# Kernel tuning notes

Measured on AMD Instinct MI355X. Metric: run time of the kernel, lower is better.

## Reference

```python
import jax, jax.numpy as jnp
import numpy as np

N_NODES = 50000
N_EDGES = 800000
NUM_GRAPHS = 64
EPS = 1e-5


def setup_inputs() -> dict:
    key = jax.random.key(0)
    ks = jax.random.split(key, 24)
    d = {}
    d['x'] = jax.random.normal(ks[0], (N_NODES, 128), dtype=jnp.float32)
    d['edge_index'] = jax.random.randint(ks[1], (2, N_EDGES), 0, N_NODES, dtype=jnp.int32)
    d['batch'] = jnp.sort(jax.random.randint(ks[2], (N_NODES,), 0, NUM_GRAPHS, dtype=jnp.int32))
    def w(k, shape, fan_in):
        return jax.random.normal(k, shape, dtype=jnp.float32) * (1.0 / np.sqrt(fan_in))
    d['W1'] = w(ks[3], (128, 256), 128)
    d['asrc1'] = w(ks[4], (4, 64), 64)
    d['adst1'] = w(ks[5], (4, 64), 64)
    d['b1'] = jnp.zeros((256,), jnp.float32)
    d['g1'] = jnp.ones((256,), jnp.float32)
    d['be1'] = jnp.zeros((256,), jnp.float32)
    d['W2'] = w(ks[6], (256, 256), 256)
    d['asrc2'] = w(ks[7], (4, 64), 64)
    d['adst2'] = w(ks[8], (4, 64), 64)
    d['b2'] = jnp.zeros((256,), jnp.float32)
    d['g2'] = jnp.ones((256,), jnp.float32)
    d['be2'] = jnp.zeros((256,), jnp.float32)
    d['W3'] = w(ks[9], (256, 128), 256)
    d['asrc3'] = w(ks[10], (1, 128), 128)
    d['adst3'] = w(ks[11], (1, 128), 128)
    d['b3'] = jnp.zeros((128,), jnp.float32)
    d['g3'] = jnp.ones((128,), jnp.float32)
    d['be3'] = jnp.zeros((128,), jnp.float32)
    d['Wp'] = w(ks[12], (256, 128), 256)
    d['bp'] = jnp.zeros((128,), jnp.float32)
    return d


def _gat(x, src, dst, W, a_src, a_dst, b, concat):
    # PyG GATConv: shared linear, per-edge additive attention, segment softmax over dst
    N = x.shape[0]
    H, C = a_src.shape
    xl = (x @ W).reshape(N, H, C)                       # [N,H,C]
    a_l = jnp.sum(xl * a_src[None], axis=-1)            # [N,H]
    a_r = jnp.sum(xl * a_dst[None], axis=-1)            # [N,H]
    e = jax.nn.leaky_relu(a_l[src] + a_r[dst], 0.2)     # [E,H]
    m = jax.ops.segment_max(e, dst, num_segments=N)
    m = jnp.where(jnp.isfinite(m), m, 0.0)
    p = jnp.exp(e - m[dst])
    s = jax.ops.segment_sum(p, dst, num_segments=N)
    alpha = p / (s[dst] + 1e-16)                        # [E,H]
    out = jax.ops.segment_sum(alpha[:, :, None] * xl[src], dst, num_segments=N)  # [N,H,C]
    out = out.reshape(N, H * C) if concat else out.mean(axis=1)
    return out + b


def _ln(x, g, b):
    mu = x.mean(-1, keepdims=True)
    var = x.var(-1, keepdims=True)
    return (x - mu) * jax.lax.rsqrt(var + EPS) * g + b


def reference(x, edge_index, batch, W1, asrc1, adst1, b1, g1, be1,
              W2, asrc2, adst2, b2, g2, be2,
              W3, asrc3, adst3, b3, g3, be3, Wp, bp):
    N = x.shape[0]
    loops = jnp.arange(N, dtype=edge_index.dtype)
    src = jnp.concatenate([edge_index[0], loops])  # add_self_loops=True
    dst = jnp.concatenate([edge_index[1], loops])
    h = jax.nn.relu(_ln(_gat(x, src, dst, W1, asrc1, adst1, b1, True), g1, be1))
    h = jax.nn.relu(_ln(_gat(h, src, dst, W2, asrc2, adst2, b2, True), g2, be2))
    h = jax.nn.relu(_ln(_gat(h, src, dst, W3, asrc3, adst3, b3, False), g3, be3))
    cnt = jax.ops.segment_sum(jnp.ones((N,), h.dtype), batch, num_segments=NUM_GRAPHS)
    h_mean = jax.ops.segment_sum(h, batch, num_segments=NUM_GRAPHS) / jnp.maximum(cnt, 1.0)[:, None]
    h_max = jax.ops.segment_max(h, batch, num_segments=NUM_GRAPHS)
    g = jnp.concatenate([h_mean, h_max], axis=-1)       # [B, 2*embed]
    return g @ Wp + bp
```

## Files before the change

kernel.cpp:

```cpp
#include <hip/hip_runtime.h>

#define EPS_LN 1e-5f
typedef unsigned int uint;

using bf16x8 = __attribute__((ext_vector_type(8))) short;
using f32x4  = __attribute__((ext_vector_type(4))) float;

__device__ inline float bf2f(ushort h){ return __uint_as_float(((uint)h) << 16); }
__device__ inline ushort f2bf(float f){
  uint u = __float_as_uint(f);
  u += 0x7fffu + ((u >> 16) & 1u);
  return (ushort)(u >> 16);
}

__global__ void k_deg(const int* __restrict__ ei, int* __restrict__ deg, int E, int N){
  int e = blockIdx.x * 256 + threadIdx.x;
  if (e >= E + N) return;
  int dst = (e < E) ? ei[E + e] : (e - E);
  atomicAdd(&deg[dst], 1);
}

__global__ __launch_bounds__(1024) void k_bsum(const int* __restrict__ deg, int* __restrict__ bsum, int n){
  __shared__ int ws[16];
  const int t = (int)threadIdx.x, lane = t & 63, w = t >> 6;
  int i = blockIdx.x * 1024 + t;
  int v = (i < n) ? deg[i] : 0;
  #pragma unroll
  for (int off = 32; off; off >>= 1) v += __shfl_xor(v, off);
  if (lane == 0) ws[w] = v;
  __syncthreads();
  if (t == 0){
    int s = 0;
    #pragma unroll
    for (int k = 0; k < 16; k++) s += ws[k];
    bsum[blockIdx.x] = s;
  }
}

__global__ __launch_bounds__(256) void k_misc(int* __restrict__ bsum, int nb,
                                              const int* __restrict__ batch, int* __restrict__ pos,
                                              int N, int G){
  const int t = (int)threadIdx.x;
  if (blockIdx.x == 0){
    if (t >= 64) return;
    const int lane = t;
    int carry = 0;
    for (int b0 = 0; b0 < nb; b0 += 64){
      int i = b0 + lane;
      int v = (i < nb) ? bsum[i] : 0;
      int s = v;
      #pragma unroll
      for (int off = 1; off < 64; off <<= 1){ int u = __shfl_up(s, off); if (lane >= off) s += u; }
      if (i < nb) bsum[i] = s - v + carry;
      carry += __shfl(s, 63);
    }
  } else {
    int g = t;
    if (g > G) return;
    int lo = 0, hi = N;
    while (lo < hi){
      int mid = (lo + hi) >> 1;
      if (batch[mid] < g) lo = mid + 1; else hi = mid;
    }
    pos[g] = lo;
  }
}

__global__ __launch_bounds__(1024) void k_scan2(const int* __restrict__ deg, const int* __restrict__ bpre,
                                                int* __restrict__ row_ptr, int* __restrict__ cursor, int n){
  __shared__ int wsum[16];
  const int t = (int)threadIdx.x, lane = t & 63, w = t >> 6;
  int i = blockIdx.x * 1024 + t;
  int v = (i < n) ? deg[i] : 0;
  int s = v;
  #pragma unroll
  for (int off = 1; off < 64; off <<= 1){ int u = __shfl_up(s, off); if (lane >= off) s += u; }
  if (lane == 63) wsum[w] = s;
  __syncthreads();
  if (w == 0 && lane < 16){
    int sc = wsum[lane];
    #pragma unroll
    for (int off = 1; off < 16; off <<= 1){ int u = __shfl_up(sc, off); if (lane >= off) sc += u; }
    wsum[lane] = sc;
  }
  __syncthreads();
  int prefix = bpre[blockIdx.x] + (w ? wsum[w - 1] : 0) + s;
  if (i < n){ row_ptr[i + 1] = prefix; cursor[i] = prefix - v; }
  if (i == 0) row_ptr[0] = 0;
}

__global__ void k_scatter(const int* __restrict__ ei, int* __restrict__ cursor,
                          int* __restrict__ csr_src, int E, int N){
  int e = blockIdx.x * 256 + threadIdx.x;
  if (e >= E + N) return;
  int src, dst;
  if (e < E){ src = ei[e]; dst = ei[E + e]; } else { src = dst = e - E; }
  int pos = atomicAdd(&cursor[dst], 1);
  csr_src[pos] = src;
}

__global__ void k_prep(const float* __restrict__ x, ushort* __restrict__ x_bf,
                       const float* __restrict__ W1, ushort* __restrict__ W1t,
                       const float* __restrict__ W2, ushort* __restrict__ W2t,
                       const float* __restrict__ W3, ushort* __restrict__ W3t, int N){
  int i = blockIdx.x * 256 + threadIdx.x;
  const int c0 = N * 32;
  if (i < c0){
    float4 v = reinterpret_cast<const float4*>(x)[i];
    ushort4 o; o.x = f2bf(v.x); o.y = f2bf(v.y); o.z = f2bf(v.z); o.w = f2bf(v.w);
    reinterpret_cast<ushort4*>(x_bf)[i] = o;
    return;
  }
  i -= c0;
  if (i < 256 * 128){
    int n = i >> 7, k = i & 127;
    W1t[i] = f2bf(W1[(size_t)k * 256 + n]);
    return;
  }
  i -= 256 * 128;
  if (i < 256 * 256){
    int n = i >> 8, k = i & 255;
    W2t[i] = f2bf(W2[(size_t)k * 256 + n]);
    return;
  }
  i -= 256 * 256;
  if (i < 128 * 256){
    int n = i >> 8, k = i & 255;
    W3t[i] = f2bf(W3[(size_t)k * 128 + n]);
  }
}

template<int K, int N, int H>
__global__ __launch_bounds__(256, 2) void k_mm(const ushort* __restrict__ A,
                                               const ushort* __restrict__ Wt,
                                               ushort* __restrict__ out,
                                               const float* __restrict__ asrc,
                                               const float* __restrict__ adst,
                                               float* __restrict__ al, float* __restrict__ ar,
                                               int M)
{
  constexpr int BANDS = (N / H) / 64;
  __shared__ __align__(16) ushort ldsA[128 * 128];
  __shared__ __align__(16) ushort ldsB[128 * 128];

  const int t = (int)threadIdx.x;
  const int lane = t & 63;
  const int w = t >> 6;
  const int wm = w >> 1, wn = w & 1;
  const int row0 = blockIdx.x * 128;
  const int n0 = blockIdx.y * 128;
  const int trow = t >> 4;
  const int tk = t & 15;

  f32x4 acc[4][4];
  #pragma unroll
  for (int mt = 0; mt < 4; mt++)
    #pragma unroll
    for (int nt = 0; nt < 4; nt++)
      acc[mt][nt] = (f32x4){0.f, 0.f, 0.f, 0.f};

  #pragma unroll
  for (int kt = 0; kt < K / 128; kt++){
    uint4 ra[8], rb[8];
    #pragma unroll
    for (int p = 0; p < 8; p++){
      int arow = p * 16 + trow;
      int grow = row0 + arow; if (grow > M - 1) grow = M - 1;
      ra[p] = *reinterpret_cast<const uint4*>(&A[(size_t)grow * K + kt * 128 + tk * 8]);
      rb[p] = *reinterpret_cast<const uint4*>(&Wt[(size_t)(n0 + arow) * K + kt * 128 + tk * 8]);
    }
    if (kt) __syncthreads();
    #pragma unroll
    for (int p = 0; p < 8; p++){
      int arow = p * 16 + trow;
      int sw = (tk ^ (arow & 7)) * 8;
      *reinterpret_cast<uint4*>(&ldsA[arow * 128 + sw]) = ra[p];
      *reinterpret_cast<uint4*>(&ldsB[arow * 128 + sw]) = rb[p];
    }
    __syncthreads();

    #pragma unroll
    for (int ks = 0; ks < 4; ks++){
      bf16x8 af[4], bfr[4];
      const int kb8 = ks * 4 + (lane >> 4);
      #pragma unroll
      for (int mt = 0; mt < 4; mt++){
        int arow = wm * 64 + mt * 16 + (lane & 15);
        af[mt] = *reinterpret_cast<const bf16x8*>(&ldsA[arow * 128 + ((kb8 ^ (arow & 7)) * 8)]);
        int brow = wn * 64 + mt * 16 + (lane & 15);
        bfr[mt] = *reinterpret_cast<const bf16x8*>(&ldsB[brow * 128 + ((kb8 ^ (brow & 7)) * 8)]);
      }
      #pragma unroll
      for (int mt = 0; mt < 4; mt++)
        #pragma unroll
        for (int nt = 0; nt < 4; nt++)
          acc[mt][nt] = __builtin_amdgcn_mfma_f32_16x16x32_bf16(af[mt], bfr[nt], acc[mt][nt], 0, 0, 0);
    }
  }

  #pragma unroll
  for (int mt = 0; mt < 4; mt++){
    const int grow_b = row0 + wm * 64 + mt * 16 + (lane >> 4) * 4;
    #pragma unroll
    for (int nt = 0; nt < 4; nt++){
      const int gcol = n0 + wn * 64 + nt * 16 + (lane & 15);
      #pragma unroll
      for (int r = 0; r < 4; r++){
        int grow = grow_b + r;
        if (grow < M) out[(size_t)grow * N + gcol] = f2bf(acc[mt][nt][r]);
      }
    }
  }

  float av[4], bv[4];
  #pragma unroll
  for (int nt = 0; nt < 4; nt++){
    int col = n0 + wn * 64 + nt * 16 + (lane & 15);
    av[nt] = asrc[col]; bv[nt] = adst[col];
  }
  float paA[4][4], pbA[4][4];
  #pragma unroll
  for (int mt = 0; mt < 4; mt++){
    #pragma unroll
    for (int r = 0; r < 4; r++){
      float pa = acc[mt][0][r] * av[0] + acc[mt][1][r] * av[1]
               + acc[mt][2][r] * av[2] + acc[mt][3][r] * av[3];
      float pb = acc[mt][0][r] * bv[0] + acc[mt][1][r] * bv[1]
               + acc[mt][2][r] * bv[2] + acc[mt][3][r] * bv[3];
      #pragma unroll
      for (int off = 1; off < 16; off <<= 1){ pa += __shfl_xor(pa, off); pb += __shfl_xor(pb, off); }
      paA[mt][r] = pa; pbA[mt][r] = pb;
    }
  }
  if constexpr (BANDS == 1){
    const int h = (n0 + wn * 64) / (N / H);
    if ((lane & 15) == 0){
      #pragma unroll
      for (int mt = 0; mt < 4; mt++){
        #pragma unroll
        for (int r = 0; r < 4; r++){
          int row = row0 + wm * 64 + mt * 16 + (lane >> 4) * 4 + r;
          if (row < M){
            al[(size_t)row * H + h] = paA[mt][r];
            ar[(size_t)row * H + h] = pbA[mt][r];
          }
        }
      }
    }
  } else {
    __syncthreads();
    float* fl = reinterpret_cast<float*>(ldsA);
    if (wn == 0 && (lane & 15) == 0){
      #pragma unroll
      for (int mt = 0; mt < 4; mt++){
        #pragma unroll
        for (int r = 0; r < 4; r++){
          int rl = wm * 64 + mt * 16 + (lane >> 4) * 4 + r;
          fl[rl] = paA[mt][r]; fl[128 + rl] = pbA[mt][r];
        }
      }
    }
    __syncthreads();
    if (wn == 1 && (lane & 15) == 0){
      #pragma unroll
      for (int mt = 0; mt < 4; mt++){
        #pragma unroll
        for (int r = 0; r < 4; r++){
          int rl = wm * 64 + mt * 16 + (lane >> 4) * 4 + r;
          int row = row0 + rl;
          if (row < M){
            al[row] = fl[rl] + paA[mt][r];
            ar[row] = fl[128 + rl] + pbA[mt][r];
          }
        }
      }
    }
  }
}

template<int DIM>
__device__ inline void gstep4(const char* __restrict__ xlb, int laneB, int s, float p, float* acc){
  uint2 v = *reinterpret_cast<const uint2*>(xlb + (size_t)((uint)s * (uint)(DIM * 2)) + laneB);
  acc[0] = fmaf(p, __uint_as_float(v.x << 16), acc[0]);
  acc[1] = fmaf(p, __uint_as_float(v.x & 0xffff0000u), acc[1]);
  acc[2] = fmaf(p, __uint_as_float(v.y << 16), acc[2]);
  acc[3] = fmaf(p, __uint_as_float(v.y & 0xffff0000u), acc[3]);
}
template<int DIM>
__device__ inline void gstep2(const char* __restrict__ xlb, int laneB, int s, float p, float* acc){
  uint v = *reinterpret_cast<const uint*>(xlb + (size_t)((uint)s * (uint)(DIM * 2)) + laneB);
  acc[0] = fmaf(p, __uint_as_float(v << 16), acc[0]);
  acc[1] = fmaf(p, __uint_as_float(v & 0xffff0000u), acc[1]);
}

template<int H, int DIM, bool BF16_OUT>
__global__ __launch_bounds__(256) void k_aggw(
    const ushort* __restrict__ xl,
    const float* __restrict__ al, const float* __restrict__ ar,
    const int* __restrict__ row_ptr, const int* __restrict__ csr_src,
    const float* __restrict__ bias, const float* __restrict__ gamma, const float* __restrict__ beta,
    float* __restrict__ out, int N)
{
  constexpr int EPL = DIM / 64;
  constexpr int PST = 68;
  const int tid = (int)threadIdx.x;
  const int wid = tid >> 6, lane = tid & 63;
  __shared__ float plds_all[4][H * PST];
  __shared__ int   slds_all[4][64];
  float* plds = plds_all[wid];
  int*   slds = slds_all[wid];
  const int n = blockIdx.x * 4 + wid;
  if (n >= N) return;
  const int start = __builtin_amdgcn_readfirstlane(row_ptr[n]);
  const int end   = __builtin_amdgcn_readfirstlane(row_ptr[n + 1]);
  const int deg   = end - start;
  const int hm    = (H == 4) ? (lane >> 4) : 0;
  const int hb    = hm * PST;
  const int laneB = lane * (EPL * 2);

  float arv[H];
  #pragma unroll
  for (int h = 0; h < H; h++) arv[h] = ar[(size_t)n * H + h];

  float acc[EPL];
  #pragma unroll
  for (int e = 0; e < EPL; e++) acc[e] = 0.f;
  float psum[H];
  const char* xlb = (const char*)xl;

  auto gather = [&](int cnt){
    int j = 0;
    for (; j + 8 <= cnt; j += 8){
      int s0 = slds[j+0], s1 = slds[j+1], s2 = slds[j+2], s3 = slds[j+3];
      int s4 = slds[j+4], s5 = slds[j+5], s6 = slds[j+6], s7 = slds[j+7];
      float q0 = plds[hb+j+0], q1 = plds[hb+j+1], q2 = plds[hb+j+2], q3 = plds[hb+j+3];
      float q4 = plds[hb+j+4], q5 = plds[hb+j+5], q6 = plds[hb+j+6], q7 = plds[hb+j+7];
      if constexpr (EPL == 4){
        gstep4<DIM>(xlb, laneB, s0, q0, acc); gstep4<DIM>(xlb, laneB, s1, q1, acc);
        gstep4<DIM>(xlb, laneB, s2, q2, acc); gstep4<DIM>(xlb, laneB, s3, q3, acc);
        gstep4<DIM>(xlb, laneB, s4, q4, acc); gstep4<DIM>(xlb, laneB, s5, q5, acc);
        gstep4<DIM>(xlb, laneB, s6, q6, acc); gstep4<DIM>(xlb, laneB, s7, q7, acc);
      } else {
        gstep2<DIM>(xlb, laneB, s0, q0, acc); gstep2<DIM>(xlb, laneB, s1, q1, acc);
        gstep2<DIM>(xlb, laneB, s2, q2, acc); gstep2<DIM>(xlb, laneB, s3, q3, acc);
        gstep2<DIM>(xlb, laneB, s4, q4, acc); gstep2<DIM>(xlb, laneB, s5, q5, acc);
        gstep2<DIM>(xlb, laneB, s6, q6, acc); gstep2<DIM>(xlb, laneB, s7, q7, acc);
      }
    }
    for (; j + 2 <= cnt; j += 2){
      int s0 = slds[j+0], s1 = slds[j+1];
      float q0 = plds[hb+j+0], q1 = plds[hb+j+1];
      if constexpr (EPL == 4){ gstep4<DIM>(xlb, laneB, s0, q0, acc); gstep4<DIM>(xlb, laneB, s1, q1, acc); }
      else                   { gstep2<DIM>(xlb, laneB, s0, q0, acc); gstep2<DIM>(xlb, laneB, s1, q1, acc); }
    }
    if (j < cnt){
      int s0 = slds[j];
      float q0 = plds[hb+j];
      if constexpr (EPL == 4) gstep4<DIM>(xlb, laneB, s0, q0, acc);
      else                    gstep2<DIM>(xlb, laneB, s0, q0, acc);
    }
  };

  if (deg <= 64){
    int src = csr_src[start + (lane < deg ? lane : deg - 1)];
    slds[lane] = src;
    float e[H];
    if constexpr (H == 4){
      float4 a4 = *reinterpret_cast<const float4*>(&al[(size_t)src * 4]);
      e[0] = a4.x + arv[0]; e[1] = a4.y + arv[1]; e[2] = a4.z + arv[2]; e[3] = a4.w + arv[3];
    } else {
      e[0] = al[src] + arv[0];
    }
    #pragma unroll
    for (int h = 0; h < H; h++){
      e[h] = e[h] > 0.f ? e[h] : 0.2f * e[h];
      if (lane >= deg) e[h] = -1e30f;
    }
    float mx[H];
    #pragma unroll
    for (int h = 0; h < H; h++){
      mx[h] = e[h];
      #pragma unroll
      for (int off = 32; off; off >>= 1) mx[h] = fmaxf(mx[h], __shfl_xor(mx[h], off));
    }
    #pragma unroll
    for (int h = 0; h < H; h++){
      float p = (lane < deg) ? __expf(e[h] - mx[h]) : 0.f;
      plds[h * PST + lane] = p;
      psum[h] = p;
      #pragma unroll
      for (int off = 32; off; off >>= 1) psum[h] += __shfl_xor(psum[h], off);
    }
    __asm__ volatile("s_waitcnt lgkmcnt(0)" ::: "memory");
    __builtin_amdgcn_wave_barrier();
    gather(deg);
  } else {
    float mx[H];
    #pragma unroll
    for (int h = 0; h < H; h++) mx[h] = -1e30f;
    for (int i = start + lane; i < end; i += 64){
      int src = csr_src[i];
      if constexpr (H == 4){
        float4 a4 = *reinterpret_cast<const float4*>(&al[(size_t)src * 4]);
        float e0 = a4.x + arv[0]; e0 = e0 > 0.f ? e0 : 0.2f * e0; mx[0] = fmaxf(mx[0], e0);
        float e1 = a4.y + arv[1]; e1 = e1 > 0.f ? e1 : 0.2f * e1; mx[1] = fmaxf(mx[1], e1);
        float e2 = a4.z + arv[2]; e2 = e2 > 0.f ? e2 : 0.2f * e2; mx[2] = fmaxf(mx[2], e2);
        float e3 = a4.w + arv[3]; e3 = e3 > 0.f ? e3 : 0.2f * e3; mx[3] = fmaxf(mx[3], e3);
      } else {
        float e = al[src] + arv[0]; e = e > 0.f ? e : 0.2f * e; mx[0] = fmaxf(mx[0], e);
      }
    }
    #pragma unroll
    for (int h = 0; h < H; h++){
      #pragma unroll
      for (int off = 32; off; off >>= 1) mx[h] = fmaxf(mx[h], __shfl_xor(mx[h], off));
    }
    #pragma unroll
    for (int h = 0; h < H; h++) psum[h] = 0.f;
    for (int c0 = start; c0 < end; c0 += 64){
      const int cnt = min(64, end - c0);
      __asm__ volatile("s_waitcnt lgkmcnt(0)" ::: "memory");
      __builtin_amdgcn_wave_barrier();
      if (lane < cnt){
        int src = csr_src[c0 + lane];
        slds[lane] = src;
        if constexpr (H == 4){
          float4 a4 = *reinterpret_cast<const float4*>(&al[(size_t)src * 4]);
          float e0 = a4.x + arv[0]; e0 = e0 > 0.f ? e0 : 0.2f * e0; float p0 = __expf(e0 - mx[0]);
          float e1 = a4.y + arv[1]; e1 = e1 > 0.f ? e1 : 0.2f * e1; float p1 = __expf(e1 - mx[1]);
          float e2 = a4.z + arv[2]; e2 = e2 > 0.f ? e2 : 0.2f * e2; float p2 = __expf(e2 - mx[2]);
          float e3 = a4.w + arv[3]; e3 = e3 > 0.f ? e3 : 0.2f * e3; float p3 = __expf(e3 - mx[3]);
          plds[0 * PST + lane] = p0; plds[1 * PST + lane] = p1;
          plds[2 * PST + lane] = p2; plds[3 * PST + lane] = p3;
          psum[0] += p0; psum[1] += p1; psum[2] += p2; psum[3] += p3;
        } else {
          float e = al[src] + arv[0]; e = e > 0.f ? e : 0.2f * e; float p = __expf(e - mx[0]);
          plds[lane] = p; psum[0] += p;
        }
      }
      __asm__ volatile("s_waitcnt lgkmcnt(0)" ::: "memory");
      __builtin_amdgcn_wave_barrier();
      gather(cnt);
    }
    #pragma unroll
    for (int h = 0; h < H; h++){
      #pragma unroll
      for (int off = 32; off; off >>= 1) psum[h] += __shfl_xor(psum[h], off);
    }
  }

  float ssel;
  if constexpr (H == 4){
    ssel = (hm == 0) ? psum[0] : (hm == 1) ? psum[1] : (hm == 2) ? psum[2] : psum[3];
  } else {
    ssel = psum[0];
  }
  const float inv = 1.f / (ssel + 1e-16f);

  float v[EPL];
  if constexpr (EPL == 4){
    float4 bb = *reinterpret_cast<const float4*>(&bias[lane * 4]);
    v[0] = fmaf(acc[0], inv, bb.x); v[1] = fmaf(acc[1], inv, bb.y);
    v[2] = fmaf(acc[2], inv, bb.z); v[3] = fmaf(acc[3], inv, bb.w);
  } else {
    float2 bb = *reinterpret_cast<const float2*>(&bias[lane * 2]);
    v[0] = fmaf(acc[0], inv, bb.x); v[1] = fmaf(acc[1], inv, bb.y);
  }
  float s1 = 0.f, s2 = 0.f;
  #pragma unroll
  for (int e = 0; e < EPL; e++){ s1 += v[e]; s2 += v[e] * v[e]; }
  #pragma unroll
  for (int off = 32; off; off >>= 1){ s1 += __shfl_xor(s1, off); s2 += __shfl_xor(s2, off); }
  const float mu = s1 / DIM;
  const float rstd = rsqrtf(s2 / DIM - mu * mu + EPS_LN);

  if constexpr (EPL == 4){
    float4 gg = *reinterpret_cast<const float4*>(&gamma[lane * 4]);
    float4 be = *reinterpret_cast<const float4*>(&beta[lane * 4]);
    float o0 = fmaxf((v[0] - mu) * rstd * gg.x + be.x, 0.f);
    float o1 = fmaxf((v[1] - mu) * rstd * gg.y + be.y, 0.f);
    float o2 = fmaxf((v[2] - mu) * rstd * gg.z + be.z, 0.f);
    float o3 = fmaxf((v[3] - mu) * rstd * gg.w + be.w, 0.f);
    if constexpr (BF16_OUT){
      uint2 pk;
      pk.x = (uint)f2bf(o0) | ((uint)f2bf(o1) << 16);
      pk.y = (uint)f2bf(o2) | ((uint)f2bf(o3) << 16);
      *reinterpret_cast<uint2*>(&reinterpret_cast<ushort*>(out)[(size_t)n * DIM + lane * 4]) = pk;
    } else {
      *reinterpret_cast<float4*>(&out[(size_t)n * DIM + lane * 4]) = make_float4(o0, o1, o2, o3);
    }
  } else {
    float2 gg = *reinterpret_cast<const float2*>(&gamma[lane * 2]);
    float2 be = *reinterpret_cast<const float2*>(&beta[lane * 2]);
    float o0 = fmaxf((v[0] - mu) * rstd * gg.x + be.x, 0.f);
    float o1 = fmaxf((v[1] - mu) * rstd * gg.y + be.y, 0.f);
    if constexpr (BF16_OUT){
      uint pk = (uint)f2bf(o0) | ((uint)f2bf(o1) << 16);
      reinterpret_cast<uint*>(out)[(size_t)n * (DIM / 2) + lane] = pk;
    } else {
      *reinterpret_cast<float2*>(&out[(size_t)n * DIM + lane * 2]) = make_float2(o0, o1);
    }
  }
}

__global__ __launch_bounds__(128) void k_pool(const float* __restrict__ h, const int* __restrict__ pos,
    float* __restrict__ pool_sum, unsigned* __restrict__ pool_max){
  const int c = (int)threadIdx.x;
  const int g = blockIdx.x >> 2;
  const int q = blockIdx.x & 3;
  const int s = pos[g], e = pos[g + 1];
  const int len = e - s;
  if (len <= 0) return;
  const int chunk = (len + 3) >> 2;
  const int n0 = s + q * chunk;
  const int n1 = min(n0 + chunk, e);
  if (n0 >= n1) return;
  float sum = 0.f, mx = 0.f;
  for (int n = n0; n < n1; n++){
    float v = h[(size_t)n * 128 + c];
    sum += v; mx = fmaxf(mx, v);
  }
  atomicAdd(&pool_sum[g * 128 + c], sum);
  atomicMax(&pool_max[g * 128 + c], __float_as_uint(mx));
}

__global__ __launch_bounds__(128) void k_final(const float* __restrict__ pool_sum,
    const unsigned* __restrict__ pool_max, const int* __restrict__ pos,
    const float* __restrict__ Wp, const float* __restrict__ bp, float* __restrict__ out){
  const int g = blockIdx.x;
  const int j = (int)threadIdx.x;
  float inv = 1.f / fmaxf((float)(pos[g + 1] - pos[g]), 1.f);
  float acc = bp[j];
  #pragma unroll 4
  for (int k = 0; k < 128; k++)
    acc = fmaf(pool_sum[g * 128 + k] * inv, Wp[k * 128 + j], acc);
  #pragma unroll 4
  for (int k = 0; k < 128; k++)
    acc = fmaf(__uint_as_float(pool_max[g * 128 + k]), Wp[(128 + k) * 128 + j], acc);
  out[g * 128 + j] = acc;
}

extern "C" void kernel_launch(void* const* d_in, const int* in_sizes, int n_in,
                              void* d_out, int out_size, void* d_ws, size_t ws_size,
                              hipStream_t stream){
  const float* x     = (const float*)d_in[0];
  const int*   ei    = (const int*)d_in[1];
  const int*   batch = (const int*)d_in[2];
  const float* W1    = (const float*)d_in[3];
  const float* asrc1 = (const float*)d_in[4];
  const float* adst1 = (const float*)d_in[5];
  const float* b1    = (const float*)d_in[6];
  const float* g1    = (const float*)d_in[7];
  const float* be1   = (const float*)d_in[8];
  const float* W2    = (const float*)d_in[9];
  const float* asrc2 = (const float*)d_in[10];
  const float* adst2 = (const float*)d_in[11];
  const float* b2    = (const float*)d_in[12];
  const float* g2    = (const float*)d_in[13];
  const float* be2   = (const float*)d_in[14];
  const float* W3    = (const float*)d_in[15];
  const float* asrc3 = (const float*)d_in[16];
  const float* adst3 = (const float*)d_in[17];
  const float* b3    = (const float*)d_in[18];
  const float* g3    = (const float*)d_in[19];
  const float* be3   = (const float*)d_in[20];
  const float* Wp    = (const float*)d_in[21];
  const float* bp    = (const float*)d_in[22];

  const int N = in_sizes[0] / 128;
  const int E = in_sizes[1] / 2;
  const int G = out_size / 128;
  const int EN = E + N;

  char* ws = (char*)d_ws;
  size_t off = 0;
  auto alloc = [&](size_t bytes) -> char* {
    char* p = ws + off;
    off = (off + bytes + 255) & ~(size_t)255;
    return p;
  };
  ushort*   region0  = (ushort*)alloc((size_t)N * 256 * 2);
  ushort*   x_bf     = region0;
  ushort*   h_bf     = region0;
  ushort*   xbufA    = (ushort*)alloc((size_t)N * 256 * 2);
  float*    xbufB    = (float*)alloc((size_t)N * 128 * 4);
  float*    al       = (float*)alloc((size_t)N * 4 * 4);
  float*    ar       = (float*)alloc((size_t)N * 4 * 4);
  int*      deg      = (int*)alloc((size_t)N * 4);
  int*      row_ptr  = (int*)alloc((size_t)(N + 1) * 4);
  int*      cursor   = (int*)alloc((size_t)N * 4);
  int*      csr_src  = (int*)alloc((size_t)EN * 4);
  int*      pos      = (int*)alloc((size_t)(G + 1) * 4);
  float*    pool_sum = (float*)alloc((size_t)G * 128 * 4);
  unsigned* pool_max = (unsigned*)alloc((size_t)G * 128 * 4);
  ushort*   W1t      = (ushort*)alloc((size_t)256 * 128 * 2);
  ushort*   W2t      = (ushort*)alloc((size_t)256 * 256 * 2);
  ushort*   W3t      = (ushort*)alloc((size_t)128 * 256 * 2);
  const int NB = (N + 1023) / 1024;
  int*      bsum     = (int*)alloc((size_t)NB * 4);

  hipMemsetAsync(deg, 0, (size_t)N * 4, stream);
  hipMemsetAsync(pool_sum, 0, (size_t)G * 128 * 4, stream);
  hipMemsetAsync(pool_max, 0, (size_t)G * 128 * 4, stream);

  k_deg<<<(EN + 255) / 256, 256, 0, stream>>>(ei, deg, E, N);
  k_bsum<<<NB, 1024, 0, stream>>>(deg, bsum, N);
  k_misc<<<2, 256, 0, stream>>>(bsum, NB, batch, pos, N, G);
  k_scan2<<<NB, 1024, 0, stream>>>(deg, bsum, row_ptr, cursor, N);
  k_scatter<<<(EN + 255) / 256, 256, 0, stream>>>(ei, cursor, csr_src, E, N);
  {
    int total = N * 32 + 256 * 128 + 256 * 256 + 128 * 256;
    k_prep<<<(total + 255) / 256, 256, 0, stream>>>(x, x_bf, W1, W1t, W2, W2t, W3, W3t, N);
  }

  const int MB = (N + 127) / 128;
  const int NB4 = (N + 3) / 4;

  k_mm<128, 256, 4><<<dim3(MB, 2), 256, 0, stream>>>(x_bf, W1t, xbufA, asrc1, adst1, al, ar, N);
  k_aggw<4, 256, true><<<NB4, 256, 0, stream>>>(xbufA, al, ar, row_ptr, csr_src, b1, g1, be1, (float*)h_bf, N);

  k_mm<256, 256, 4><<<dim3(MB, 2), 256, 0, stream>>>(h_bf, W2t, xbufA, asrc2, adst2, al, ar, N);
  k_aggw<4, 256, true><<<NB4, 256, 0, stream>>>(xbufA, al, ar, row_ptr, csr_src, b2, g2, be2, (float*)h_bf, N);

  k_mm<256, 128, 1><<<dim3(MB, 1), 256, 0, stream>>>(h_bf, W3t, xbufA, asrc3, adst3, al, ar, N);
  k_aggw<1, 128, false><<<NB4, 256, 0, stream>>>(xbufA, al, ar, row_ptr, csr_src, b3, g3, be3, xbufB, N);

  k_pool<<<G * 4, 128, 0, stream>>>(xbufB, pos, pool_sum, pool_max);
  k_final<<<G, 128, 0, stream>>>(pool_sum, pool_max, pos, Wp, bp, (float*)d_out);
}
```

Before: 462.5 us.

## Merge preprocessing launches, use single-pass decoupled scan, fuse pooling with final linear

```diff
diff --git a/kernel.cpp b/kernel.cpp
--- a/kernel.cpp
+++ b/kernel.cpp
@@ -13,64 +13,72 @@
   return (ushort)(u >> 16);
 }
 
-__global__ void k_deg(const int* __restrict__ ei, int* __restrict__ deg, int E, int N){
-  int e = blockIdx.x * 256 + threadIdx.x;
-  if (e >= E + N) return;
-  int dst = (e < E) ? ei[E + e] : (e - E);
-  atomicAdd(&deg[dst], 1);
-}
-
-__global__ __launch_bounds__(1024) void k_bsum(const int* __restrict__ deg, int* __restrict__ bsum, int n){
-  __shared__ int ws[16];
+__global__ void k_prep(const float* __restrict__ x, ushort* __restrict__ x_bf,
+                       const float* __restrict__ W1, ushort* __restrict__ W1t,
+                       const float* __restrict__ W2, ushort* __restrict__ W2t,
+                       const float* __restrict__ W3, ushort* __restrict__ W3t,
+                       const int* __restrict__ ei, int* __restrict__ deg,
+                       const int* __restrict__ batch, int* __restrict__ pos,
+                       float* __restrict__ pool_sum, uint* __restrict__ pool_max,
+                       int* __restrict__ done, int* __restrict__ flag,
+                       int N, int E, int G, int NB){
+  int i = blockIdx.x * 256 + threadIdx.x;
+  const int c0 = N * 32;
+  if (i < c0){
+    float4 v = reinterpret_cast<const float4*>(x)[i];
+    ushort4 o; o.x = f2bf(v.x); o.y = f2bf(v.y); o.z = f2bf(v.z); o.w = f2bf(v.w);
+    reinterpret_cast<ushort4*>(x_bf)[i] = o;
+    return;
+  }
+  i -= c0;
+  if (i < 256 * 128){
+    int n = i >> 7, k = i & 127;
+    W1t[i] = f2bf(W1[(size_t)k * 256 + n]);
+    return;
+  }
+  i -= 256 * 128;
+  if (i < 256 * 256){
+    int n = i >> 8, k = i & 255;
+    W2t[i] = f2bf(W2[(size_t)k * 256 + n]);
+    return;
+  }
+  i -= 256 * 256;
+  if (i < 128 * 256){
+    int n = i >> 8, k = i & 255;
+    W3t[i] = f2bf(W3[(size_t)k * 128 + n]);
+    return;
+  }
+  i -= 128 * 256;
+  if (i < E + N){
+    int dst = (i < E) ? ei[E + i] : (i - E);
+    atomicAdd(&deg[dst], 1);
+    return;
+  }
+  i -= E + N;
+  if (i < G * 128){
+    pool_sum[i] = 0.f;
+    pool_max[i] = 0u;
+    if (i < G) done[i] = 0;
+    if (i < NB) flag[i] = 0;
+    if (i <= G){
+      int lo = 0, hi = N;
+      while (lo < hi){
+        int mid = (lo + hi) >> 1;
+        if (batch[mid] < i) lo = mid + 1; else hi = mid;
+      }
+      pos[i] = lo;
+    }
+  }
+}
+
+__global__ __launch_bounds__(1024) void k_scanall(const int* __restrict__ deg,
+    int* __restrict__ row_ptr, int* __restrict__ cursor,
+    int* __restrict__ pref, int* __restrict__ flag, int n){
+  __shared__ int wsum[16];
+  __shared__ int prev_s;
+  const int b = (int)blockIdx.x;
   const int t = (int)threadIdx.x, lane = t & 63, w = t >> 6;
-  int i = blockIdx.x * 1024 + t;
-  int v = (i < n) ? deg[i] : 0;
-  #pragma unroll
-  for (int off = 32; off; off >>= 1) v += __shfl_xor(v, off);
-  if (lane == 0) ws[w] = v;
-  __syncthreads();
-  if (t == 0){
-    int s = 0;
-    #pragma unroll
-    for (int k = 0; k < 16; k++) s += ws[k];
-    bsum[blockIdx.x] = s;
-  }
-}
-
-__global__ __launch_bounds__(256) void k_misc(int* __restrict__ bsum, int nb,
-                                              const int* __restrict__ batch, int* __restrict__ pos,
-                                              int N, int G){
-  const int t = (int)threadIdx.x;
-  if (blockIdx.x == 0){
-    if (t >= 64) return;
-    const int lane = t;
-    int carry = 0;
-    for (int b0 = 0; b0 < nb; b0 += 64){
-      int i = b0 + lane;
-      int v = (i < nb) ? bsum[i] : 0;
-      int s = v;
-      #pragma unroll
-      for (int off = 1; off < 64; off <<= 1){ int u = __shfl_up(s, off); if (lane >= off) s += u; }
-      if (i < nb) bsum[i] = s - v + carry;
-      carry += __shfl(s, 63);
-    }
-  } else {
-    int g = t;
-    if (g > G) return;
-    int lo = 0, hi = N;
-    while (lo < hi){
-      int mid = (lo + hi) >> 1;
-      if (batch[mid] < g) lo = mid + 1; else hi = mid;
-    }
-    pos[g] = lo;
-  }
-}
-
-__global__ __launch_bounds__(1024) void k_scan2(const int* __restrict__ deg, const int* __restrict__ bpre,
-                                                int* __restrict__ row_ptr, int* __restrict__ cursor, int n){
-  __shared__ int wsum[16];
-  const int t = (int)threadIdx.x, lane = t & 63, w = t >> 6;
-  int i = blockIdx.x * 1024 + t;
+  int i = b * 1024 + t;
   int v = (i < n) ? deg[i] : 0;
   int s = v;
   #pragma unroll
@@ -84,7 +92,21 @@
     wsum[lane] = sc;
   }
   __syncthreads();
-  int prefix = bpre[blockIdx.x] + (w ? wsum[w - 1] : 0) + s;
+  const int local_inc = (w ? wsum[w - 1] : 0) + s;
+  if (t == 0){
+    int prev = 0;
+    if (b > 0){
+      while (atomicCAS(&flag[b - 1], 1, 1) == 0){}
+      __threadfence();
+      prev = pref[b - 1];
+    }
+    pref[b] = prev + wsum[15];
+    __threadfence();
+    atomicExch(&flag[b], 1);
+    prev_s = prev;
+  }
+  __syncthreads();
+  const int prefix = prev_s + local_inc;
   if (i < n){ row_ptr[i + 1] = prefix; cursor[i] = prefix - v; }
   if (i == 0) row_ptr[0] = 0;
 }
@@ -97,37 +119,6 @@
   if (e < E){ src = ei[e]; dst = ei[E + e]; } else { src = dst = e - E; }
   int pos = atomicAdd(&cursor[dst], 1);
   csr_src[pos] = src;
-}
-
-__global__ void k_prep(const float* __restrict__ x, ushort* __restrict__ x_bf,
-                       const float* __restrict__ W1, ushort* __restrict__ W1t,
-                       const float* __restrict__ W2, ushort* __restrict__ W2t,
-                       const float* __restrict__ W3, ushort* __restrict__ W3t, int N){
-  int i = blockIdx.x * 256 + threadIdx.x;
-  const int c0 = N * 32;
-  if (i < c0){
-    float4 v = reinterpret_cast<const float4*>(x)[i];
-    ushort4 o; o.x = f2bf(v.x); o.y = f2bf(v.y); o.z = f2bf(v.z); o.w = f2bf(v.w);
-    reinterpret_cast<ushort4*>(x_bf)[i] = o;
-    return;
-  }
-  i -= c0;
-  if (i < 256 * 128){
-    int n = i >> 7, k = i & 127;
-    W1t[i] = f2bf(W1[(size_t)k * 256 + n]);
-    return;
-  }
-  i -= 256 * 128;
-  if (i < 256 * 256){
-    int n = i >> 8, k = i & 255;
-    W2t[i] = f2bf(W2[(size_t)k * 256 + n]);
-    return;
-  }
-  i -= 256 * 256;
-  if (i < 128 * 256){
-    int n = i >> 8, k = i & 255;
-    W3t[i] = f2bf(W3[(size_t)k * 128 + n]);
-  }
 }
 
 template<int K, int N, int H>
@@ -503,41 +494,45 @@
   }
 }
 
-__global__ __launch_bounds__(128) void k_pool(const float* __restrict__ h, const int* __restrict__ pos,
-    float* __restrict__ pool_sum, unsigned* __restrict__ pool_max){
+__global__ __launch_bounds__(128) void k_poolfin(const float* __restrict__ h, const int* __restrict__ pos,
+    float* __restrict__ pool_sum, uint* __restrict__ pool_max, int* __restrict__ done,
+    const float* __restrict__ Wp, const float* __restrict__ bp, float* __restrict__ out){
   const int c = (int)threadIdx.x;
   const int g = blockIdx.x >> 2;
   const int q = blockIdx.x & 3;
   const int s = pos[g], e = pos[g + 1];
   const int len = e - s;
-  if (len <= 0) return;
-  const int chunk = (len + 3) >> 2;
-  const int n0 = s + q * chunk;
-  const int n1 = min(n0 + chunk, e);
-  if (n0 >= n1) return;
-  float sum = 0.f, mx = 0.f;
-  for (int n = n0; n < n1; n++){
-    float v = h[(size_t)n * 128 + c];
-    sum += v; mx = fmaxf(mx, v);
-  }
-  atomicAdd(&pool_sum[g * 128 + c], sum);
-  atomicMax(&pool_max[g * 128 + c], __float_as_uint(mx));
-}
-
-__global__ __launch_bounds__(128) void k_final(const float* __restrict__ pool_sum,
-    const unsigned* __restrict__ pool_max, const int* __restrict__ pos,
-    const float* __restrict__ Wp, const float* __restrict__ bp, float* __restrict__ out){
-  const int g = blockIdx.x;
-  const int j = (int)threadIdx.x;
-  float inv = 1.f / fmaxf((float)(pos[g + 1] - pos[g]), 1.f);
-  float acc = bp[j];
-  #pragma unroll 4
-  for (int k = 0; k < 128; k++)
-    acc = fmaf(pool_sum[g * 128 + k] * inv, Wp[k * 128 + j], acc);
-  #pragma unroll 4
-  for (int k = 0; k < 128; k++)
-    acc = fmaf(__uint_as_float(pool_max[g * 128 + k]), Wp[(128 + k) * 128 + j], acc);
-  out[g * 128 + j] = acc;
+  if (len > 0){
+    const int chunk = (len + 3) >> 2;
+    const int n0 = s + q * chunk;
+    const int n1 = min(n0 + chunk, e);
+    if (n0 < n1){
+      float sum = 0.f, mx = 0.f;
+      for (int n = n0; n < n1; n++){
+        float v = h[(size_t)n * 128 + c];
+        sum += v; mx = fmaxf(mx, v);
+      }
+      atomicAdd(&pool_sum[g * 128 + c], sum);
+      atomicMax(&pool_max[g * 128 + c], __float_as_uint(mx));
+    }
+  }
+  __threadfence();
+  __syncthreads();
+  __shared__ int old_s;
+  if (c == 0) old_s = atomicAdd(&done[g], 1);
+  __syncthreads();
+  if (old_s == 3){
+    __threadfence();
+    float inv = 1.f / fmaxf((float)len, 1.f);
+    float acc = bp[c];
+    #pragma unroll 4
+    for (int k = 0; k < 128; k++)
+      acc = fmaf(pool_sum[g * 128 + k] * inv, Wp[k * 128 + c], acc);
+    #pragma unroll 4
+    for (int k = 0; k < 128; k++)
+      acc = fmaf(__uint_as_float(pool_max[g * 128 + k]), Wp[(128 + k) * 128 + c], acc);
+    out[g * 128 + c] = acc;
+  }
 }
 
 extern "C" void kernel_launch(void* const* d_in, const int* in_sizes, int n_in,
@@ -592,26 +587,26 @@
   int*      csr_src  = (int*)alloc((size_t)EN * 4);
   int*      pos      = (int*)alloc((size_t)(G + 1) * 4);
   float*    pool_sum = (float*)alloc((size_t)G * 128 * 4);
-  unsigned* pool_max = (unsigned*)alloc((size_t)G * 128 * 4);
+  uint*     pool_max = (uint*)alloc((size_t)G * 128 * 4);
+  int*      done     = (int*)alloc((size_t)G * 4);
   ushort*   W1t      = (ushort*)alloc((size_t)256 * 128 * 2);
   ushort*   W2t      = (ushort*)alloc((size_t)256 * 256 * 2);
   ushort*   W3t      = (ushort*)alloc((size_t)128 * 256 * 2);
   const int NB = (N + 1023) / 1024;
-  int*      bsum     = (int*)alloc((size_t)NB * 4);
+  int*      pref     = (int*)alloc((size_t)NB * 4);
+  int*      flag     = (int*)alloc((size_t)NB * 4);
 
   hipMemsetAsync(deg, 0, (size_t)N * 4, stream);
-  hipMemsetAsync(pool_sum, 0, (size_t)G * 128 * 4, stream);
-  hipMemsetAsync(pool_max, 0, (size_t)G * 128 * 4, stream);
-
-  k_deg<<<(EN + 255) / 256, 256, 0, stream>>>(ei, deg, E, N);
-  k_bsum<<<NB, 1024, 0, stream>>>(deg, bsum, N);
-  k_misc<<<2, 256, 0, stream>>>(bsum, NB, batch, pos, N, G);
-  k_scan2<<<NB, 1024, 0, stream>>>(deg, bsum, row_ptr, cursor, N);
+
+  {
+    int total = N * 32 + 256 * 128 + 256 * 256 + 128 * 256 + EN + G * 128;
+    k_prep<<<(total + 255) / 256, 256, 0, stream>>>(x, x_bf, W1, W1t, W2, W2t, W3, W3t,
+                                                    ei, deg, batch, pos,
+                                                    pool_sum, pool_max, done, flag,
+                                                    N, E, G, NB);
+  }
+  k_scanall<<<NB, 1024, 0, stream>>>(deg, row_ptr, cursor, pref, flag, N);
   k_scatter<<<(EN + 255) / 256, 256, 0, stream>>>(ei, cursor, csr_src, E, N);
-  {
-    int total = N * 32 + 256 * 128 + 256 * 256 + 128 * 256;
-    k_prep<<<(total + 255) / 256, 256, 0, stream>>>(x, x_bf, W1, W1t, W2, W2t, W3, W3t, N);
-  }
 
   const int MB = (N + 127) / 128;
   const int NB4 = (N + 3) / 4;
@@ -625,6 +620,5 @@
   k_mm<256, 128, 1><<<dim3(MB, 1), 256, 0, stream>>>(h_bf, W3t, xbufA, asrc3, adst3, al, ar, N);
   k_aggw<1, 128, false><<<NB4, 256, 0, stream>>>(xbufA, al, ar, row_ptr, csr_src, b3, g3, be3, xbufB, N);
 
-  k_pool<<<G * 4, 128, 0, stream>>>(xbufB, pos, pool_sum, pool_max);
-  k_final<<<G, 128, 0, stream>>>(pool_sum, pool_max, pos, Wp, bp, (float*)d_out);
-}
+  k_poolfin<<<G * 4, 128, 0, stream>>>(xbufB, pos, pool_sum, pool_max, done, Wp, bp, (float*)d_out);
+}
```

Result: slower. 508.8 us (+10.0%).
